# Kernel optimization log

Measured on AMD Instinct MI355X. Metric: run time of the kernel, lower is better.

The kernel has to match this reference:

```python
import jax, jax.numpy as jnp
import numpy as np

B = 131072   # batch (tokens)
D = 512      # d_model
P = 10       # n_programs
H = D // 4   # extractor hidden
MAXO = 4     # max operands
MAXR = 3     # max results


def setup_inputs() -> dict:
    key = jax.random.key(0)
    ks = jax.random.split(key, 6)
    hidden = jax.random.normal(ks[0], (B, D), jnp.float32)
    program_ids = jax.random.randint(ks[1], (B,), 0, P)
    Wr = jax.random.normal(ks[2], (D, P), jnp.float32) * (1.0 / np.sqrt(D))
    br = jnp.zeros((P,), jnp.float32)
    # stacked per-program extractor MLPs, output padded to MAXO (extra cols unused)
    W1 = jax.random.normal(ks[3], (P, D, H), jnp.float32) * (1.0 / np.sqrt(D))
    b1 = jnp.zeros((P, H), jnp.float32)
    W2 = jax.random.normal(ks[4], (P, H, MAXO), jnp.float32) * (1.0 / np.sqrt(H))
    b2 = jnp.zeros((P, MAXO), jnp.float32)
    return {"hidden": hidden, "program_ids": program_ids, "Wr": Wr, "br": br,
            "W1": W1, "b1": b1, "W2": W2, "b2": b2}


def _time_decompose(total_minutes):
    days = jnp.floor(total_minutes / 1440.0)
    rem = total_minutes - days * 1440.0
    hours = jnp.floor(rem / 60.0)
    minutes = rem - hours * 60.0
    return hours, minutes, days


def _safe(b):
    # avoid NaN/Inf from zero denominators in Mod/FloorDiv
    return jnp.where(b == 0, 1.0, b)


def _programs():
    # (fn -> tuple of result arrays, n_operands), order matches DEFAULT_PROGRAMS
    return [
        (lambda a, b: (a + b,), 2),                                   # IntAdd
        (lambda a, b: (a - b,), 2),                                   # IntSub
        (lambda a, b: (a * b,), 2),                                   # IntMul
        (lambda a, b: (jnp.mod(a, _safe(b)),), 2),                    # Mod
        (lambda a, b: (jnp.floor(a / _safe(b)),), 2),                 # FloorDiv
        (lambda h1, m1, h2, m2: _time_decompose(h1 * 60 + m1 + h2 * 60 + m2), 4),          # TimeAdd
        (lambda h1, m1, h2, m2: _time_decompose(h1 * 60 + m1 - (h2 * 60 + m2)), 4),        # TimeSub
        (lambda h1, m1, h2, m2: _time_decompose(jnp.abs(h1 * 60 + m1 - (h2 * 60 + m2))), 4),  # DurationBetween
        (lambda a, b: ((a > b).astype(jnp.float32),), 2),             # Greater
        (lambda a, b: ((a == b).astype(jnp.float32),), 2),            # Equal
    ]


def _compute_results(ops_rounded):
    # ops_rounded: [P, B, MAXO] -> results_all [P, B, MAXR]
    outs = []
    for idx, (fn, nop) in enumerate(_programs()):
        args = [ops_rounded[idx, :, i] for i in range(nop)]
        res = fn(*args)
        cols = list(res) + [jnp.zeros_like(res[0])] * (MAXR - len(res))
        outs.append(jnp.stack(cols, axis=-1))  # [B, MAXR]
    return jnp.stack(outs, axis=0)  # [P, B, MAXR]


def reference(hidden, program_ids, Wr, br, W1, b1, W2, b2):
    router_logits = hidden @ Wr + br                                  # [B, P]
    pre = jnp.einsum('bd,pdh->pbh', hidden, W1) + b1[:, None, :]      # [P, B, H]
    ops = jnp.einsum('pbh,pho->pbo', jax.nn.gelu(pre, approximate=False), W2) + b2[:, None, :]  # [P, B, MAXO]
    ops_rounded = jnp.round(ops)  # round_ste forward = round
    results_all = _compute_results(ops_rounded)                       # [P, B, MAXR]
    # combine: each row takes the result of its own program (masked scatter in torch)
    results = results_all[program_ids, jnp.arange(hidden.shape[0])]   # [B, MAXR]
    results = jax.lax.stop_gradient(results)  # torch .detach()
    return results, router_logits, ops, program_ids
```

## Files before the change

### kernel.cpp

```cpp
#include <hip/hip_runtime.h>
#include <math.h>

constexpr int D_   = 512;
constexpr int H_   = 128;
constexpr int P_   = 10;
constexpr int MAXO = 4;
constexpr int BM   = 128;
constexpr int BK   = 32;

typedef _Float16 f16;
typedef f16 f16x4 __attribute__((ext_vector_type(4)));
typedef f16 f16x8 __attribute__((ext_vector_type(8)));
typedef float f32x4 __attribute__((ext_vector_type(4)));

__device__ __forceinline__ float gelu_exact(float x) {
    return 0.5f * x * (1.0f + erff(x * 0.70710678118654752f));
}

__device__ __forceinline__ void time_decomp(float t, float& hr, float& mi, float& dy) {
    float days = floorf(t / 1440.0f);
    float rem  = t - days * 1440.0f;
    float hours = floorf(rem / 60.0f);
    float minutes = rem - hours * 60.0f;
    hr = hours; mi = minutes; dy = days;
}

__device__ __forceinline__ void g2l16(const f16* g, f16* l) {
    __builtin_amdgcn_global_load_lds(
        (const __attribute__((address_space(1))) void*)g,
        (__attribute__((address_space(3))) void*)l, 16, 0, 0);
}

__global__ __launch_bounds__(256) void cvt_w1_kernel(
    const float* __restrict__ W1, f16* __restrict__ hi, f16* __restrict__ lo)
{
    int i = blockIdx.x * 256 + threadIdx.x;
    float x = W1[i];
    f16 h = (f16)x;
    f16 L = (f16)(x - (float)h);
    int dh = i % (D_ * H_);
    int p  = i / (D_ * H_);
    int d  = dh / H_;
    int hh = dh % H_;
    size_t o = ((size_t)(p * H_ + hh)) * D_ + d;
    hi[o] = h; lo[o] = L;
}

__global__ __launch_bounds__(256) void extractor_kernel(
    const float* __restrict__ hidden,
    const int*   __restrict__ pids,
    const f16*   __restrict__ W1Thi,
    const f16*   __restrict__ W1Tlo,
    const float* __restrict__ b1,
    const float* __restrict__ W2,
    const float* __restrict__ b2,
    float* __restrict__ out_results,
    float* __restrict__ out_ops,
    int B)
{
    __shared__ f16 Ahi[BM * BK], Alo[BM * BK];
    __shared__ f16 Bhi[H_ * BK], Blo[H_ * BK];
    __shared__ float W2s[H_ * 4];
    __shared__ float red[2][BM][4];

    const int bid  = blockIdx.x;
    const int p    = bid % P_;
    const int b0   = (bid / P_) * BM;
    const int tid  = threadIdx.x;
    const int l    = tid & 63;
    const int w    = tid >> 6;
    const int wm   = w >> 1, wn = w & 1;
    const int l15  = l & 15, l4 = l >> 4;

    if (tid < H_) {
        ((f32x4*)W2s)[tid] = ((const f32x4*)(W2 + (size_t)p * H_ * 4))[tid];
    }

    f32x4 acc[4][4];
#pragma unroll
    for (int mi = 0; mi < 4; ++mi)
#pragma unroll
        for (int ni = 0; ni < 4; ++ni) acc[mi][ni] = (f32x4){0.f, 0.f, 0.f, 0.f};

    const f16* Bhig = W1Thi + (size_t)p * H_ * D_;
    const f16* Blog = W1Tlo + (size_t)p * H_ * D_;

    for (int kc = 0; kc < D_ / BK; ++kc) {
        __syncthreads();

#pragma unroll
        for (int t = 0; t < 2; ++t) {
            int h0 = w * 32 + t * 16;
            size_t ge = (size_t)(h0 + (l >> 2)) * D_ + kc * BK + (l & 3) * 8;
            g2l16(Bhig + ge, &Bhi[h0 * BK]);
            g2l16(Blog + ge, &Blo[h0 * BK]);
        }

#pragma unroll
        for (int it = 0; it < 4; ++it) {
            int i  = tid + it * 256;
            int m  = i >> 3;
            int k4 = (i & 7) * 4;
            f32x4 v = *(const f32x4*)(hidden + (size_t)(b0 + m) * D_ + kc * BK + k4);
            f16x4 vh, vl;
#pragma unroll
            for (int j = 0; j < 4; ++j) {
                f16 hj = (f16)v[j];
                vh[j] = hj;
                vl[j] = (f16)(v[j] - (float)hj);
            }
            *(f16x4*)&Ahi[m * BK + k4] = vh;
            *(f16x4*)&Alo[m * BK + k4] = vl;
        }
        __syncthreads();

        f16x8 bh[4], bl[4];
#pragma unroll
        for (int ni = 0; ni < 4; ++ni) {
            int hrow = wn * 64 + ni * 16 + l15;
            bh[ni] = *(const f16x8*)&Bhi[hrow * BK + l4 * 8];
            bl[ni] = *(const f16x8*)&Blo[hrow * BK + l4 * 8];
        }
#pragma unroll
        for (int mi = 0; mi < 4; ++mi) {
            int mrow = wm * 64 + mi * 16 + l15;
            f16x8 a_h = *(const f16x8*)&Ahi[mrow * BK + l4 * 8];
            f16x8 a_l = *(const f16x8*)&Alo[mrow * BK + l4 * 8];
#pragma unroll
            for (int ni = 0; ni < 4; ++ni) {
                acc[mi][ni] = __builtin_amdgcn_mfma_f32_16x16x32_f16(a_l, bh[ni], acc[mi][ni], 0, 0, 0);
                acc[mi][ni] = __builtin_amdgcn_mfma_f32_16x16x32_f16(a_h, bl[ni], acc[mi][ni], 0, 0, 0);
                acc[mi][ni] = __builtin_amdgcn_mfma_f32_16x16x32_f16(a_h, bh[ni], acc[mi][ni], 0, 0, 0);
            }
        }
    }

    float b1v[4];
#pragma unroll
    for (int ni = 0; ni < 4; ++ni)
        b1v[ni] = b1[p * H_ + wn * 64 + ni * 16 + l15];

#pragma unroll
    for (int mi = 0; mi < 4; ++mi) {
        float po[4][4];
#pragma unroll
        for (int r = 0; r < 4; ++r)
#pragma unroll
            for (int o = 0; o < 4; ++o) po[r][o] = 0.0f;

#pragma unroll
        for (int ni = 0; ni < 4; ++ni) {
            int h = wn * 64 + ni * 16 + l15;
            f32x4 w4 = ((const f32x4*)W2s)[h];
#pragma unroll
            for (int r = 0; r < 4; ++r) {
                float g = gelu_exact(acc[mi][ni][r] + b1v[ni]);
#pragma unroll
                for (int o = 0; o < 4; ++o) po[r][o] = fmaf(g, w4[o], po[r][o]);
            }
        }
#pragma unroll
        for (int off = 1; off < 16; off <<= 1) {
#pragma unroll
            for (int r = 0; r < 4; ++r)
#pragma unroll
                for (int o = 0; o < 4; ++o)
                    po[r][o] += __shfl_xor(po[r][o], off, 64);
        }
        float v = po[0][0];
#pragma unroll
        for (int rr = 0; rr < 4; ++rr)
#pragma unroll
            for (int oo = 0; oo < 4; ++oo)
                if (l15 == rr * 4 + oo) v = po[rr][oo];
        red[wn][wm * 64 + mi * 16 + l4 * 4 + (l15 >> 2)][l15 & 3] = v;
    }
    __syncthreads();

    if (tid < BM) {
        int b = b0 + tid;
        float o0 = red[0][tid][0] + red[1][tid][0] + b2[p * 4 + 0];
        float o1 = red[0][tid][1] + red[1][tid][1] + b2[p * 4 + 1];
        float o2 = red[0][tid][2] + red[1][tid][2] + b2[p * 4 + 2];
        float o3 = red[0][tid][3] + red[1][tid][3] + b2[p * 4 + 3];
        *reinterpret_cast<float4*>(out_ops + ((size_t)p * B + b) * MAXO) =
            make_float4(o0, o1, o2, o3);

        if (pids[b] == p) {
            float a0 = rintf(o0), a1 = rintf(o1), a2 = rintf(o2), a3 = rintf(o3);
            float r0 = 0.0f, r1 = 0.0f, r2 = 0.0f;
            switch (p) {
                case 0: r0 = a0 + a1; break;
                case 1: r0 = a0 - a1; break;
                case 2: r0 = a0 * a1; break;
                case 3: {
                    float bs = (a1 == 0.0f) ? 1.0f : a1;
                    float m = fmodf(a0, bs);
                    if (m != 0.0f && ((m < 0.0f) != (bs < 0.0f))) m += bs;
                    r0 = m;
                } break;
                case 4: {
                    float bs = (a1 == 0.0f) ? 1.0f : a1;
                    r0 = floorf(a0 / bs);
                } break;
                case 5: { float t = a0 * 60.0f + a1 + a2 * 60.0f + a3; time_decomp(t, r0, r1, r2); } break;
                case 6: { float t = a0 * 60.0f + a1 - (a2 * 60.0f + a3); time_decomp(t, r0, r1, r2); } break;
                case 7: { float t = fabsf(a0 * 60.0f + a1 - (a2 * 60.0f + a3)); time_decomp(t, r0, r1, r2); } break;
                case 8: r0 = (a0 > a1) ? 1.0f : 0.0f; break;
                case 9: r0 = (a0 == a1) ? 1.0f : 0.0f; break;
            }
            size_t ob = (size_t)b * 3;
            out_results[ob + 0] = r0;
            out_results[ob + 1] = r1;
            out_results[ob + 2] = r2;
        }
    }
}

__global__ __launch_bounds__(256) void router_kernel(
    const float* __restrict__ hidden, const float* __restrict__ Wr,
    const float* __restrict__ br, const int* __restrict__ pids,
    float* __restrict__ out_router, float* __restrict__ out_pids, int B)
{
    __shared__ float Wrs[D_ * 12];
    const int tid = threadIdx.x;
    for (int i = tid; i < D_ * P_; i += 256) {
        int k = i / P_;
        int q = i - k * P_;
        Wrs[k * 12 + q] = Wr[i];
    }
    __syncthreads();

    const int lane = tid & 63;
    const int wv   = tid >> 6;
    const int b    = blockIdx.x * 4 + wv;
    const float* hrow = hidden + (size_t)b * D_;

    float acc[P_];
#pragma unroll
    for (int q = 0; q < P_; ++q) acc[q] = 0.0f;

#pragma unroll
    for (int j = 0; j < 8; ++j) {
        int k = j * 64 + lane;
        float hv = hrow[k];
        float wv12[12];
        *reinterpret_cast<float4*>(&wv12[0]) = *reinterpret_cast<const float4*>(&Wrs[k * 12 + 0]);
        *reinterpret_cast<float4*>(&wv12[4]) = *reinterpret_cast<const float4*>(&Wrs[k * 12 + 4]);
        *reinterpret_cast<float2*>(&wv12[8]) = *reinterpret_cast<const float2*>(&Wrs[k * 12 + 8]);
#pragma unroll
        for (int q = 0; q < P_; ++q) acc[q] = fmaf(hv, wv12[q], acc[q]);
    }

#pragma unroll
    for (int off = 1; off < 64; off <<= 1) {
#pragma unroll
        for (int q = 0; q < P_; ++q)
            acc[q] += __shfl_xor(acc[q], off, 64);
    }

    if (lane == 0) {
        float* o = out_router + (size_t)b * P_;
#pragma unroll
        for (int q = 0; q < P_; ++q) o[q] = acc[q] + br[q];
        out_pids[b] = (float)pids[b];
    }
}

extern "C" void kernel_launch(void* const* d_in, const int* in_sizes, int n_in,
                              void* d_out, int out_size, void* d_ws, size_t ws_size,
                              hipStream_t stream) {
    const float* hidden = (const float*)d_in[0];
    const int*   pids   = (const int*)  d_in[1];
    const float* Wr     = (const float*)d_in[2];
    const float* br     = (const float*)d_in[3];
    const float* W1     = (const float*)d_in[4];
    const float* b1     = (const float*)d_in[5];
    const float* W2     = (const float*)d_in[6];
    const float* b2     = (const float*)d_in[7];

    const int B = in_sizes[1];

    float* out         = (float*)d_out;
    float* out_results = out;
    float* out_router  = out + (size_t)B * 3;
    float* out_ops     = out + (size_t)B * 13;
    float* out_pids    = out + (size_t)B * 13 + (size_t)P_ * B * MAXO;

    f16* W1Thi = (f16*)d_ws;
    f16* W1Tlo = W1Thi + (size_t)P_ * H_ * D_;

    cvt_w1_kernel<<<(P_ * D_ * H_) / 256, 256, 0, stream>>>(W1, W1Thi, W1Tlo);

    extractor_kernel<<<(B / BM) * P_, 256, 0, stream>>>(
        hidden, pids, W1Thi, W1Tlo, b1, W2, b2, out_results, out_ops, B);

    router_kernel<<<B / 4, 256, 0, stream>>>(hidden, Wr, br, pids,
                                             out_router, out_pids, B);
}
```

Baseline: 913.7 us.

## Pre-split hidden to fp16 hi/lo and run second MLP layer on MFMA

Adds a pre-pass that converts hidden into fp16 hi/lo halves once, so each of the ten per-program blocks loads them with async global-to-LDS copies instead of repeating the split conversion. It also replaces the scalar GELU·W2 FMA and shuffle reduction with an MFMA over GELU values staged in shared memory, using a packed hi/lo pattern matrix for W2. This removes redundant conversion work and shuffle-heavy epilogue code. In exchange it adds an extra pass writing 2×B×D fp16 to workspace, more shared memory per block (lower occupancy), and several extra barriers. The fallback path is used when the workspace is too small.

```diff
diff --git a/kernel.cpp b/kernel.cpp
--- a/kernel.cpp
+++ b/kernel.cpp
@@ -7,6 +7,7 @@
 constexpr int MAXO = 4;
 constexpr int BM   = 128;
 constexpr int BK   = 32;
+constexpr int PATW = 264;
 
 typedef _Float16 f16;
 typedef f16 f16x4 __attribute__((ext_vector_type(4)));
@@ -46,8 +47,27 @@
     hi[o] = h; lo[o] = L;
 }
 
+__global__ __launch_bounds__(256) void cvt_hidden_kernel(
+    const float* __restrict__ hidden, f16* __restrict__ hi, f16* __restrict__ lo)
+{
+    size_t i = ((size_t)blockIdx.x * 256 + threadIdx.x) * 8;
+    f32x4 v0 = *(const f32x4*)(hidden + i);
+    f32x4 v1 = *(const f32x4*)(hidden + i + 4);
+    f16x8 vh, vl;
+#pragma unroll
+    for (int j = 0; j < 4; ++j) {
+        f16 h0 = (f16)v0[j]; vh[j] = h0; vl[j] = (f16)(v0[j] - (float)h0);
+        f16 h1 = (f16)v1[j]; vh[j + 4] = h1; vl[j + 4] = (f16)(v1[j] - (float)h1);
+    }
+    *(f16x8*)(hi + i) = vh;
+    *(f16x8*)(lo + i) = vl;
+}
+
+template <bool PRECONV>
 __global__ __launch_bounds__(256) void extractor_kernel(
     const float* __restrict__ hidden,
+    const f16*   __restrict__ hidHi,
+    const f16*   __restrict__ hidLo,
     const int*   __restrict__ pids,
     const f16*   __restrict__ W1Thi,
     const f16*   __restrict__ W1Tlo,
@@ -58,10 +78,13 @@
     float* __restrict__ out_ops,
     int B)
 {
-    __shared__ f16 Ahi[BM * BK], Alo[BM * BK];
-    __shared__ f16 Bhi[H_ * BK], Blo[H_ * BK];
-    __shared__ float W2s[H_ * 4];
-    __shared__ float red[2][BM][4];
+    __shared__ __align__(16) char smem[49664];
+    f16* Ahi = (f16*)(smem);
+    f16* Alo = (f16*)(smem + 8192);
+    f16* Bhi = (f16*)(smem + 16384);
+    f16* Blo = (f16*)(smem + 24576);
+    f16* Pat = (f16*)(smem + 32768);
+    f16* Gs  = (f16*)(smem);
 
     const int bid  = blockIdx.x;
     const int p    = bid % P_;
@@ -72,8 +95,21 @@
     const int wm   = w >> 1, wn = w & 1;
     const int l15  = l & 15, l4 = l >> 4;
 
-    if (tid < H_) {
-        ((f32x4*)W2s)[tid] = ((const f32x4*)(W2 + (size_t)p * H_ * 4))[tid];
+#pragma unroll
+    for (int j = 0; j < 32; ++j) {
+        int i = tid + j * 256;
+        int pass = i >> 12;
+        int rem  = i & 4095;
+        int n    = rem >> 8;
+        int k    = rem & 255;
+        f16 val = (f16)0.f;
+        if (n < MAXO) {
+            float x = W2[(size_t)p * H_ * MAXO + (k >> 1) * MAXO + n];
+            f16 hi = (f16)x;
+            if (pass == 0) val = hi;
+            else if (!(k & 1)) val = (f16)(x - (float)hi);
+        }
+        Pat[(pass * 16 + n) * PATW + k] = val;
     }
 
     f32x4 acc[4][4];
@@ -96,21 +132,31 @@
             g2l16(Blog + ge, &Blo[h0 * BK]);
         }
 
-#pragma unroll
-        for (int it = 0; it < 4; ++it) {
-            int i  = tid + it * 256;
-            int m  = i >> 3;
-            int k4 = (i & 7) * 4;
-            f32x4 v = *(const f32x4*)(hidden + (size_t)(b0 + m) * D_ + kc * BK + k4);
-            f16x4 vh, vl;
-#pragma unroll
-            for (int j = 0; j < 4; ++j) {
-                f16 hj = (f16)v[j];
-                vh[j] = hj;
-                vl[j] = (f16)(v[j] - (float)hj);
-            }
-            *(f16x4*)&Ahi[m * BK + k4] = vh;
-            *(f16x4*)&Alo[m * BK + k4] = vl;
+        if (PRECONV) {
+#pragma unroll
+            for (int t = 0; t < 2; ++t) {
+                int m0 = w * 32 + t * 16;
+                size_t ge = (size_t)(b0 + m0 + (l >> 2)) * D_ + kc * BK + (l & 3) * 8;
+                g2l16(hidHi + ge, &Ahi[m0 * BK]);
+                g2l16(hidLo + ge, &Alo[m0 * BK]);
+            }
+        } else {
+#pragma unroll
+            for (int it = 0; it < 4; ++it) {
+                int i  = tid + it * 256;
+                int m  = i >> 3;
+                int k4 = (i & 7) * 4;
+                f32x4 v = *(const f32x4*)(hidden + (size_t)(b0 + m) * D_ + kc * BK + k4);
+                f16x4 vh, vl;
+#pragma unroll
+                for (int j = 0; j < 4; ++j) {
+                    f16 hj = (f16)v[j];
+                    vh[j] = hj;
+                    vl[j] = (f16)(v[j] - (float)hj);
+                }
+                *(f16x4*)&Ahi[m * BK + k4] = vh;
+                *(f16x4*)&Alo[m * BK + k4] = vl;
+            }
         }
         __syncthreads();
 
@@ -139,80 +185,81 @@
 #pragma unroll
     for (int ni = 0; ni < 4; ++ni)
         b1v[ni] = b1[p * H_ + wn * 64 + ni * 16 + l15];
-
-#pragma unroll
-    for (int mi = 0; mi < 4; ++mi) {
-        float po[4][4];
-#pragma unroll
-        for (int r = 0; r < 4; ++r)
-#pragma unroll
-            for (int o = 0; o < 4; ++o) po[r][o] = 0.0f;
-
-#pragma unroll
-        for (int ni = 0; ni < 4; ++ni) {
-            int h = wn * 64 + ni * 16 + l15;
-            f32x4 w4 = ((const f32x4*)W2s)[h];
+    const float b2v = b2[p * 4 + (l15 & 3)];
+
+#pragma unroll
+    for (int q = 0; q < 4; ++q) {
+        __syncthreads();
+        if (wm == (q >> 1)) {
+#pragma unroll
+            for (int s = 0; s < 2; ++s) {
+                const int mi = (q & 1) * 2 + s;
+#pragma unroll
+                for (int ni = 0; ni < 4; ++ni) {
+                    int h = wn * 64 + ni * 16 + l15;
+#pragma unroll
+                    for (int r = 0; r < 4; ++r) {
+                        int row = s * 16 + l4 * 4 + r;
+                        float g = gelu_exact(acc[mi][ni][r] + b1v[ni]);
+                        f16 gh = (f16)g;
+                        f16 gl = (f16)(g - (float)gh);
+                        unsigned int u = (unsigned int)__builtin_bit_cast(unsigned short, gh)
+                                       | ((unsigned int)__builtin_bit_cast(unsigned short, gl) << 16);
+                        ((unsigned int*)Gs)[row * (PATW / 2) + h] = u;
+                    }
+                }
+            }
+        }
+        __syncthreads();
+        if (wm != (q >> 1)) {
+            const int t = wn;
+            f32x4 c2 = (f32x4){0.f, 0.f, 0.f, 0.f};
+#pragma unroll
+            for (int kst = 0; kst < 8; ++kst) {
+                f16x8 a  = *(const f16x8*)&Gs[(t * 16 + l15) * PATW + kst * 32 + l4 * 8];
+                f16x8 p1 = *(const f16x8*)&Pat[(0 * 16 + l15) * PATW + kst * 32 + l4 * 8];
+                f16x8 p2 = *(const f16x8*)&Pat[(1 * 16 + l15) * PATW + kst * 32 + l4 * 8];
+                c2 = __builtin_amdgcn_mfma_f32_16x16x32_f16(a, p1, c2, 0, 0, 0);
+                c2 = __builtin_amdgcn_mfma_f32_16x16x32_f16(a, p2, c2, 0, 0, 0);
+            }
 #pragma unroll
             for (int r = 0; r < 4; ++r) {
-                float g = gelu_exact(acc[mi][ni][r] + b1v[ni]);
-#pragma unroll
-                for (int o = 0; o < 4; ++o) po[r][o] = fmaf(g, w4[o], po[r][o]);
-            }
-        }
-#pragma unroll
-        for (int off = 1; off < 16; off <<= 1) {
-#pragma unroll
-            for (int r = 0; r < 4; ++r)
-#pragma unroll
-                for (int o = 0; o < 4; ++o)
-                    po[r][o] += __shfl_xor(po[r][o], off, 64);
-        }
-        float v = po[0][0];
-#pragma unroll
-        for (int rr = 0; rr < 4; ++rr)
-#pragma unroll
-            for (int oo = 0; oo < 4; ++oo)
-                if (l15 == rr * 4 + oo) v = po[rr][oo];
-        red[wn][wm * 64 + mi * 16 + l4 * 4 + (l15 >> 2)][l15 & 3] = v;
-    }
-    __syncthreads();
-
-    if (tid < BM) {
-        int b = b0 + tid;
-        float o0 = red[0][tid][0] + red[1][tid][0] + b2[p * 4 + 0];
-        float o1 = red[0][tid][1] + red[1][tid][1] + b2[p * 4 + 1];
-        float o2 = red[0][tid][2] + red[1][tid][2] + b2[p * 4 + 2];
-        float o3 = red[0][tid][3] + red[1][tid][3] + b2[p * 4 + 3];
-        *reinterpret_cast<float4*>(out_ops + ((size_t)p * B + b) * MAXO) =
-            make_float4(o0, o1, o2, o3);
-
-        if (pids[b] == p) {
-            float a0 = rintf(o0), a1 = rintf(o1), a2 = rintf(o2), a3 = rintf(o3);
-            float r0 = 0.0f, r1 = 0.0f, r2 = 0.0f;
-            switch (p) {
-                case 0: r0 = a0 + a1; break;
-                case 1: r0 = a0 - a1; break;
-                case 2: r0 = a0 * a1; break;
-                case 3: {
-                    float bs = (a1 == 0.0f) ? 1.0f : a1;
-                    float m = fmodf(a0, bs);
-                    if (m != 0.0f && ((m < 0.0f) != (bs < 0.0f))) m += bs;
-                    r0 = m;
-                } break;
-                case 4: {
-                    float bs = (a1 == 0.0f) ? 1.0f : a1;
-                    r0 = floorf(a0 / bs);
-                } break;
-                case 5: { float t = a0 * 60.0f + a1 + a2 * 60.0f + a3; time_decomp(t, r0, r1, r2); } break;
-                case 6: { float t = a0 * 60.0f + a1 - (a2 * 60.0f + a3); time_decomp(t, r0, r1, r2); } break;
-                case 7: { float t = fabsf(a0 * 60.0f + a1 - (a2 * 60.0f + a3)); time_decomp(t, r0, r1, r2); } break;
-                case 8: r0 = (a0 > a1) ? 1.0f : 0.0f; break;
-                case 9: r0 = (a0 == a1) ? 1.0f : 0.0f; break;
-            }
-            size_t ob = (size_t)b * 3;
-            out_results[ob + 0] = r0;
-            out_results[ob + 1] = r1;
-            out_results[ob + 2] = r2;
+                int tok = b0 + q * 32 + t * 16 + l4 * 4 + r;
+                float vr = c2[r] + b2v;
+                float v1 = __shfl_xor(vr, 1, 64);
+                float v2 = __shfl_xor(vr, 2, 64);
+                float v3 = __shfl_xor(vr, 3, 64);
+                if (l15 < 4)
+                    out_ops[((size_t)p * B + tok) * MAXO + l15] = vr;
+                if (l15 == 0 && pids[tok] == p) {
+                    float a0 = rintf(vr), a1 = rintf(v1), a2 = rintf(v2), a3 = rintf(v3);
+                    float r0 = 0.0f, r1 = 0.0f, r2 = 0.0f;
+                    switch (p) {
+                        case 0: r0 = a0 + a1; break;
+                        case 1: r0 = a0 - a1; break;
+                        case 2: r0 = a0 * a1; break;
+                        case 3: {
+                            float bs = (a1 == 0.0f) ? 1.0f : a1;
+                            float m = fmodf(a0, bs);
+                            if (m != 0.0f && ((m < 0.0f) != (bs < 0.0f))) m += bs;
+                            r0 = m;
+                        } break;
+                        case 4: {
+                            float bs = (a1 == 0.0f) ? 1.0f : a1;
+                            r0 = floorf(a0 / bs);
+                        } break;
+                        case 5: { float tt = a0 * 60.0f + a1 + a2 * 60.0f + a3; time_decomp(tt, r0, r1, r2); } break;
+                        case 6: { float tt = a0 * 60.0f + a1 - (a2 * 60.0f + a3); time_decomp(tt, r0, r1, r2); } break;
+                        case 7: { float tt = fabsf(a0 * 60.0f + a1 - (a2 * 60.0f + a3)); time_decomp(tt, r0, r1, r2); } break;
+                        case 8: r0 = (a0 > a1) ? 1.0f : 0.0f; break;
+                        case 9: r0 = (a0 == a1) ? 1.0f : 0.0f; break;
+                    }
+                    size_t ob = (size_t)tok * 3;
+                    out_results[ob + 0] = r0;
+                    out_results[ob + 1] = r1;
+                    out_results[ob + 2] = r2;
+                }
+            }
         }
     }
 }
@@ -287,13 +334,27 @@
     float* out_ops     = out + (size_t)B * 13;
     float* out_pids    = out + (size_t)B * 13 + (size_t)P_ * B * MAXO;
 
+    const size_t nW1  = (size_t)P_ * H_ * D_;
+    const size_t nHid = (size_t)B * D_;
+    const size_t need = (2 * nW1 + 2 * nHid) * sizeof(f16);
+
     f16* W1Thi = (f16*)d_ws;
-    f16* W1Tlo = W1Thi + (size_t)P_ * H_ * D_;
-
-    cvt_w1_kernel<<<(P_ * D_ * H_) / 256, 256, 0, stream>>>(W1, W1Thi, W1Tlo);
-
-    extractor_kernel<<<(B / BM) * P_, 256, 0, stream>>>(
-        hidden, pids, W1Thi, W1Tlo, b1, W2, b2, out_results, out_ops, B);
+    f16* W1Tlo = W1Thi + nW1;
+
+    cvt_w1_kernel<<<(int)(nW1 / 256), 256, 0, stream>>>(W1, W1Thi, W1Tlo);
+
+    if (ws_size >= need) {
+        f16* hidHi = W1Tlo + nW1;
+        f16* hidLo = hidHi + nHid;
+        cvt_hidden_kernel<<<(int)(nHid / (256 * 8)), 256, 0, stream>>>(hidden, hidHi, hidLo);
+        extractor_kernel<true><<<(B / BM) * P_, 256, 0, stream>>>(
+            hidden, hidHi, hidLo, pids, W1Thi, W1Tlo, b1, W2, b2,
+            out_results, out_ops, B);
+    } else {
+        extractor_kernel<false><<<(B / BM) * P_, 256, 0, stream>>>(
+            hidden, nullptr, nullptr, pids, W1Thi, W1Tlo, b1, W2, b2,
+            out_results, out_ops, B);
+    }
 
     router_kernel<<<B / 4, 256, 0, stream>>>(hidden, Wr, br, pids,
                                              out_router, out_pids, B);
```

New measurement: 1.637 ms. 1.79x slower.

## Double-buffer extractor LDS tiles, preconvert hidden to fp16 split, remap blocks

Applied to the files above, without the earlier changes.

Adds a pre-pass that splits hidden into fp16 hi/lo arrays once, so the extractor no longer repeats the fp32 load and split for each of the 10 programs. The extractor now loads A through async global-to-LDS copies and double-buffers the A and B tiles, overlapping loads with MFMA work and halving the barriers per K step. Block indices are remapped in groups of 8 to change which row-groups and programs run together, aiming for better cache locality. The cost is an extra full read and write of hidden, a larger workspace, and about 70KB of LDS per block, which may lower occupancy.

```diff
diff --git a/kernel.cpp b/kernel.cpp
--- a/kernel.cpp
+++ b/kernel.cpp
@@ -46,8 +46,27 @@
     hi[o] = h; lo[o] = L;
 }
 
+__global__ __launch_bounds__(256) void cvt_hidden_kernel(
+    const float* __restrict__ hidden, f16* __restrict__ hi, f16* __restrict__ lo)
+{
+    size_t i = ((size_t)blockIdx.x * 256 + threadIdx.x) * 8;
+    f32x4 v0 = *(const f32x4*)(hidden + i);
+    f32x4 v1 = *(const f32x4*)(hidden + i + 4);
+    f16x8 vh, vl;
+#pragma unroll
+    for (int j = 0; j < 4; ++j) {
+        f16 h0 = (f16)v0[j]; vh[j] = h0; vl[j] = (f16)(v0[j] - (float)h0);
+        f16 h1 = (f16)v1[j]; vh[j + 4] = h1; vl[j + 4] = (f16)(v1[j] - (float)h1);
+    }
+    *(f16x8*)(hi + i) = vh;
+    *(f16x8*)(lo + i) = vl;
+}
+
+template <bool PRECONV>
 __global__ __launch_bounds__(256) void extractor_kernel(
     const float* __restrict__ hidden,
+    const f16*   __restrict__ hidHi,
+    const f16*   __restrict__ hidLo,
     const int*   __restrict__ pids,
     const f16*   __restrict__ W1Thi,
     const f16*   __restrict__ W1Tlo,
@@ -58,19 +77,37 @@
     float* __restrict__ out_ops,
     int B)
 {
-    __shared__ f16 Ahi[BM * BK], Alo[BM * BK];
-    __shared__ f16 Bhi[H_ * BK], Blo[H_ * BK];
-    __shared__ float W2s[H_ * 4];
-    __shared__ float red[2][BM][4];
-
-    const int bid  = blockIdx.x;
-    const int p    = bid % P_;
-    const int b0   = (bid / P_) * BM;
-    const int tid  = threadIdx.x;
-    const int l    = tid & 63;
-    const int w    = tid >> 6;
-    const int wm   = w >> 1, wn = w & 1;
-    const int l15  = l & 15, l4 = l >> 4;
+    __shared__ __align__(16) char smem[71680];
+    f16* A0h = (f16*)(smem);
+    f16* A0l = (f16*)(smem + 8192);
+    f16* B0h = (f16*)(smem + 16384);
+    f16* B0l = (f16*)(smem + 24576);
+    f16* A1h = (f16*)(smem + 32768);
+    f16* A1l = (f16*)(smem + 40960);
+    f16* B1h = (f16*)(smem + 49152);
+    f16* B1l = (f16*)(smem + 57344);
+    float* red = (float*)(smem + 65536);
+    float* W2s = (float*)(smem + 69632);
+
+    const int bid = blockIdx.x;
+    const int ngroups = gridDim.x / P_;
+    int g, p;
+    if ((ngroups & 7) == 0) {
+        const int gpx = ngroups >> 3;
+        const int x   = bid & 7;
+        const int q   = bid >> 3;
+        g = x * gpx + q / P_;
+        p = q % P_;
+    } else {
+        g = bid / P_;
+        p = bid % P_;
+    }
+    const int b0  = g * BM;
+    const int tid = threadIdx.x;
+    const int l   = tid & 63;
+    const int w   = tid >> 6;
+    const int wm  = w >> 1, wn = w & 1;
+    const int l15 = l & 15, l4 = l >> 4;
 
     if (tid < H_) {
         ((f32x4*)W2s)[tid] = ((const f32x4*)(W2 + (size_t)p * H_ * 4))[tid];
@@ -85,47 +122,56 @@
     const f16* Bhig = W1Thi + (size_t)p * H_ * D_;
     const f16* Blog = W1Tlo + (size_t)p * H_ * D_;
 
-    for (int kc = 0; kc < D_ / BK; ++kc) {
-        __syncthreads();
-
+    auto stageB = [&](int kc, f16* Bh, f16* Bl) {
 #pragma unroll
         for (int t = 0; t < 2; ++t) {
             int h0 = w * 32 + t * 16;
-            size_t ge = (size_t)(h0 + (l >> 2)) * D_ + kc * BK + (l & 3) * 8;
-            g2l16(Bhig + ge, &Bhi[h0 * BK]);
-            g2l16(Blog + ge, &Blo[h0 * BK]);
-        }
-
-#pragma unroll
-        for (int it = 0; it < 4; ++it) {
-            int i  = tid + it * 256;
-            int m  = i >> 3;
-            int k4 = (i & 7) * 4;
-            f32x4 v = *(const f32x4*)(hidden + (size_t)(b0 + m) * D_ + kc * BK + k4);
-            f16x4 vh, vl;
-#pragma unroll
-            for (int j = 0; j < 4; ++j) {
-                f16 hj = (f16)v[j];
-                vh[j] = hj;
-                vl[j] = (f16)(v[j] - (float)hj);
-            }
-            *(f16x4*)&Ahi[m * BK + k4] = vh;
-            *(f16x4*)&Alo[m * BK + k4] = vl;
-        }
-        __syncthreads();
-
+            size_t go = (size_t)(h0 + (l >> 2)) * D_ + kc * BK + (l & 3) * 8;
+            g2l16(Bhig + go, Bh + h0 * BK);
+            g2l16(Blog + go, Bl + h0 * BK);
+        }
+    };
+    auto stageA = [&](int kc, f16* Ah, f16* Al) {
+        if constexpr (PRECONV) {
+#pragma unroll
+            for (int t = 0; t < 2; ++t) {
+                int m0 = w * 32 + t * 16;
+                size_t ga = (size_t)(b0 + m0 + (l >> 2)) * D_ + kc * BK + (l & 3) * 8;
+                g2l16(hidHi + ga, Ah + m0 * BK);
+                g2l16(hidLo + ga, Al + m0 * BK);
+            }
+        } else {
+#pragma unroll
+            for (int it = 0; it < 4; ++it) {
+                int i  = tid + it * 256;
+                int m  = i >> 3;
+                int k4 = (i & 7) * 4;
+                f32x4 v = *(const f32x4*)(hidden + (size_t)(b0 + m) * D_ + kc * BK + k4);
+                f16x4 vh, vl;
+#pragma unroll
+                for (int j = 0; j < 4; ++j) {
+                    f16 hj = (f16)v[j];
+                    vh[j] = hj;
+                    vl[j] = (f16)(v[j] - (float)hj);
+                }
+                *(f16x4*)&Ah[m * BK + k4] = vh;
+                *(f16x4*)&Al[m * BK + k4] = vl;
+            }
+        }
+    };
+    auto compute = [&](const f16* Ah, const f16* Al, const f16* Bh, const f16* Bl) {
         f16x8 bh[4], bl[4];
 #pragma unroll
         for (int ni = 0; ni < 4; ++ni) {
             int hrow = wn * 64 + ni * 16 + l15;
-            bh[ni] = *(const f16x8*)&Bhi[hrow * BK + l4 * 8];
-            bl[ni] = *(const f16x8*)&Blo[hrow * BK + l4 * 8];
+            bh[ni] = *(const f16x8*)&Bh[hrow * BK + l4 * 8];
+            bl[ni] = *(const f16x8*)&Bl[hrow * BK + l4 * 8];
         }
 #pragma unroll
         for (int mi = 0; mi < 4; ++mi) {
             int mrow = wm * 64 + mi * 16 + l15;
-            f16x8 a_h = *(const f16x8*)&Ahi[mrow * BK + l4 * 8];
-            f16x8 a_l = *(const f16x8*)&Alo[mrow * BK + l4 * 8];
+            f16x8 a_h = *(const f16x8*)&Ah[mrow * BK + l4 * 8];
+            f16x8 a_l = *(const f16x8*)&Al[mrow * BK + l4 * 8];
 #pragma unroll
             for (int ni = 0; ni < 4; ++ni) {
                 acc[mi][ni] = __builtin_amdgcn_mfma_f32_16x16x32_f16(a_l, bh[ni], acc[mi][ni], 0, 0, 0);
@@ -133,6 +179,22 @@
                 acc[mi][ni] = __builtin_amdgcn_mfma_f32_16x16x32_f16(a_h, bh[ni], acc[mi][ni], 0, 0, 0);
             }
         }
+    };
+
+    stageA(0, A0h, A0l);
+    stageB(0, B0h, B0l);
+    __syncthreads();
+    for (int kc = 0; kc < 16; kc += 2) {
+        stageA(kc + 1, A1h, A1l);
+        stageB(kc + 1, B1h, B1l);
+        compute(A0h, A0l, B0h, B0l);
+        __syncthreads();
+        if (kc + 2 < 16) {
+            stageA(kc + 2, A0h, A0l);
+            stageB(kc + 2, B0h, B0l);
+        }
+        compute(A1h, A1l, B1h, B1l);
+        __syncthreads();
     }
 
     float b1v[4];
@@ -154,9 +216,9 @@
             f32x4 w4 = ((const f32x4*)W2s)[h];
 #pragma unroll
             for (int r = 0; r < 4; ++r) {
-                float g = gelu_exact(acc[mi][ni][r] + b1v[ni]);
-#pragma unroll
-                for (int o = 0; o < 4; ++o) po[r][o] = fmaf(g, w4[o], po[r][o]);
+                float gg = gelu_exact(acc[mi][ni][r] + b1v[ni]);
+#pragma unroll
+                for (int o = 0; o < 4; ++o) po[r][o] = fmaf(gg, w4[o], po[r][o]);
             }
         }
 #pragma unroll
@@ -173,16 +235,18 @@
 #pragma unroll
             for (int oo = 0; oo < 4; ++oo)
                 if (l15 == rr * 4 + oo) v = po[rr][oo];
-        red[wn][wm * 64 + mi * 16 + l4 * 4 + (l15 >> 2)][l15 & 3] = v;
+        red[(wn * 128 + wm * 64 + mi * 16 + l4 * 4 + (l15 >> 2)) * 4 + (l15 & 3)] = v;
     }
     __syncthreads();
 
     if (tid < BM) {
         int b = b0 + tid;
-        float o0 = red[0][tid][0] + red[1][tid][0] + b2[p * 4 + 0];
-        float o1 = red[0][tid][1] + red[1][tid][1] + b2[p * 4 + 1];
-        float o2 = red[0][tid][2] + red[1][tid][2] + b2[p * 4 + 2];
-        float o3 = red[0][tid][3] + red[1][tid][3] + b2[p * 4 + 3];
+        const float* r0p = &red[(0 * 128 + tid) * 4];
+        const float* r1p = &red[(1 * 128 + tid) * 4];
+        float o0 = r0p[0] + r1p[0] + b2[p * 4 + 0];
+        float o1 = r0p[1] + r1p[1] + b2[p * 4 + 1];
+        float o2 = r0p[2] + r1p[2] + b2[p * 4 + 2];
+        float o3 = r0p[3] + r1p[3] + b2[p * 4 + 3];
         *reinterpret_cast<float4*>(out_ops + ((size_t)p * B + b) * MAXO) =
             make_float4(o0, o1, o2, o3);
 
@@ -203,9 +267,9 @@
                     float bs = (a1 == 0.0f) ? 1.0f : a1;
                     r0 = floorf(a0 / bs);
                 } break;
-                case 5: { float t = a0 * 60.0f + a1 + a2 * 60.0f + a3; time_decomp(t, r0, r1, r2); } break;
-                case 6: { float t = a0 * 60.0f + a1 - (a2 * 60.0f + a3); time_decomp(t, r0, r1, r2); } break;
-                case 7: { float t = fabsf(a0 * 60.0f + a1 - (a2 * 60.0f + a3)); time_decomp(t, r0, r1, r2); } break;
+                case 5: { float tt = a0 * 60.0f + a1 + a2 * 60.0f + a3; time_decomp(tt, r0, r1, r2); } break;
+                case 6: { float tt = a0 * 60.0f + a1 - (a2 * 60.0f + a3); time_decomp(tt, r0, r1, r2); } break;
+                case 7: { float tt = fabsf(a0 * 60.0f + a1 - (a2 * 60.0f + a3)); time_decomp(tt, r0, r1, r2); } break;
                 case 8: r0 = (a0 > a1) ? 1.0f : 0.0f; break;
                 case 9: r0 = (a0 == a1) ? 1.0f : 0.0f; break;
             }
@@ -287,13 +351,27 @@
     float* out_ops     = out + (size_t)B * 13;
     float* out_pids    = out + (size_t)B * 13 + (size_t)P_ * B * MAXO;
 
+    const size_t nW1  = (size_t)P_ * H_ * D_;
+    const size_t nHid = (size_t)B * D_;
+    const size_t need = (2 * nW1 + 2 * nHid) * sizeof(f16);
+
     f16* W1Thi = (f16*)d_ws;
-    f16* W1Tlo = W1Thi + (size_t)P_ * H_ * D_;
-
-    cvt_w1_kernel<<<(P_ * D_ * H_) / 256, 256, 0, stream>>>(W1, W1Thi, W1Tlo);
-
-    extractor_kernel<<<(B / BM) * P_, 256, 0, stream>>>(
-        hidden, pids, W1Thi, W1Tlo, b1, W2, b2, out_results, out_ops, B);
+    f16* W1Tlo = W1Thi + nW1;
+
+    cvt_w1_kernel<<<(int)(nW1 / 256), 256, 0, stream>>>(W1, W1Thi, W1Tlo);
+
+    if (ws_size >= need) {
+        f16* hidHi = W1Tlo + nW1;
+        f16* hidLo = hidHi + nHid;
+        cvt_hidden_kernel<<<(int)(nHid / (256 * 8)), 256, 0, stream>>>(hidden, hidHi, hidLo);
+        extractor_kernel<true><<<(B / BM) * P_, 256, 0, stream>>>(
+            hidden, hidHi, hidLo, pids, W1Thi, W1Tlo, b1, W2, b2,
+            out_results, out_ops, B);
+    } else {
+        extractor_kernel<false><<<(B / BM) * P_, 256, 0, stream>>>(
+            hidden, nullptr, nullptr, pids, W1Thi, W1Tlo, b1, W2, b2,
+            out_results, out_ops, B);
+    }
 
     router_kernel<<<B / 4, 256, 0, stream>>>(hidden, Wr, br, pids,
                                              out_router, out_pids, B);
```

Measured after the change: 883.6 us. -3.3%, faster.
